# Kernel optimization log

Hardware: AMD Instinct MI355X
Metric: run time of the kernel (lower is better)

The kernel has to match this reference:

```python
import jax, jax.numpy as jnp
import numpy as np

B, N, DIM = 2, 2048, 1024
H, DH = 16, 64
DIM_INNER = H * DH
EPS = float(jnp.finfo(jnp.float32).eps)  # torch nn.RMSNorm default eps = finfo.eps
THETA = 10000.0


def setup_inputs() -> dict:
    key = jax.random.key(0)
    ks = jax.random.split(key, 6)
    s = 0.02
    tokens = jax.random.normal(ks[0], (B, N, DIM), dtype=jnp.float32)
    w_norm = jnp.ones((DIM,), jnp.float32)                      # prenorm RMSNorm weight
    w_q = jax.random.normal(ks[1], (DIM, DIM_INNER), jnp.float32) * s
    w_k = jax.random.normal(ks[2], (DIM, 3 * DIM_INNER), jnp.float32) * s
    w_v = jax.random.normal(ks[3], (DIM, 3 * DIM_INNER), jnp.float32) * s
    w_key_norms = jnp.ones((3, DH), jnp.float32)                # 3 key RMSNorms
    w_nested_knorm = jnp.ones((DH,), jnp.float32)
    w_out = jax.random.normal(ks[4], (DIM_INNER, DIM), jnp.float32) * s
    return {"tokens": tokens, "w_norm": w_norm, "w_q": w_q, "w_k": w_k,
            "w_v": w_v, "w_key_norms": w_key_norms,
            "w_nested_knorm": w_nested_knorm, "w_out": w_out}


def rmsnorm(x, w):
    var = jnp.mean(jnp.square(x), axis=-1, keepdims=True)
    return x * jax.lax.rsqrt(var + EPS) * w


def rope(x):
    # interleaved (GPT-J style) rotary, as in rotary_embedding_torch defaults
    n, d = x.shape[-2], x.shape[-1]
    inv_freq = 1.0 / (THETA ** (jnp.arange(0, d, 2, dtype=jnp.float32) / d))
    freqs = jnp.arange(n, dtype=jnp.float32)[:, None] * inv_freq   # (n, d/2)
    cos = jnp.repeat(jnp.cos(freqs), 2, axis=-1)                   # (n, d)
    sin = jnp.repeat(jnp.sin(freqs), 2, axis=-1)
    x1, x2 = x[..., ::2], x[..., 1::2]
    x_rot = jnp.stack((-x2, x1), axis=-1).reshape(x.shape)         # rotate_half
    return x * cos + x_rot * sin


def attend(q, k, v):
    # rotate_queries_with_cached_keys with equal lengths -> plain rotary on both
    q = rope(q)
    k = rope(k)
    d = q.shape[-1]
    scores = jnp.einsum('bhqd,bhkd->bhqk', q, k) / jnp.sqrt(jnp.float32(d))
    n = scores.shape[-1]
    causal = jnp.tril(jnp.ones((n, n), dtype=bool))
    scores = jnp.where(causal, scores, -jnp.inf)
    attn = jax.nn.softmax(scores, axis=-1)
    return jnp.einsum('bhqk,bhkd->bhqd', attn, v)


def reference(tokens, w_norm, w_q, w_k, w_v, w_key_norms, w_nested_knorm, w_out):
    b, n = tokens.shape[:2]
    x = rmsnorm(tokens, w_norm)                                    # prenorm
    q = (x @ w_q).reshape(b, n, H, DH).transpose(0, 2, 1, 3)       # (b,h,n,d)
    # chunk(3, dim=-1) then split heads -> (3,b,h,n,d)
    ks = (x @ w_k).reshape(b, n, 3, H, DH).transpose(2, 0, 3, 1, 4)
    vs = (x @ w_v).reshape(b, n, 3, H, DH).transpose(2, 0, 3, 1, 4)
    ks = rmsnorm(ks, w_key_norms[:, None, None, None, :])          # per-branch key norm
    # three parallel causal attentions sharing the same queries
    nq, nk, nv = jax.vmap(attend, in_axes=(None, 0, 0))(q, ks, vs)
    nk = rmsnorm(nk, w_nested_knorm)
    out = attend(nq, nk, nv)                                       # nested attention
    out = out.transpose(0, 2, 1, 3).reshape(b, n, DIM_INNER)       # merge heads
    return out @ w_out
```

## Files before the change

kernel.cpp:

```cpp
#include <hip/hip_runtime.h>
#include <hip/hip_bf16.h>
#include <stdint.h>

typedef unsigned short u16;
typedef __attribute__((ext_vector_type(8))) short short8;
typedef __attribute__((ext_vector_type(4))) float float4v;
typedef __attribute__((ext_vector_type(4))) unsigned int uint4v;

#define B_    2
#define N_    2048
#define DIM_  1024
#define H_    16
#define DH_   64
#define DI_   1024
#define EPS_  1.1920928955078125e-07f
#define LOG2_THETA 13.287712379549449f
#define SCL_  0.18033688011112042f

__device__ __forceinline__ float bf2f(u16 u) {
    union { unsigned int i; float f; } v; v.i = ((unsigned int)u) << 16; return v.f;
}
__device__ __forceinline__ u16 f2bf(float f) {
    union { float f; unsigned int i; } v; v.f = f;
    unsigned int r = v.i + 0x7fff + ((v.i >> 16) & 1);
    return (u16)(r >> 16);
}
__device__ __forceinline__ unsigned int cvtpk(float a, float b) {
    unsigned int r;
    asm("v_cvt_pk_bf16_f32 %0, %1, %2" : "=v"(r) : "v"(a), "v"(b));
    return r;
}
__device__ __forceinline__ int perm32(int n) {
    return (n & ~31) + (((n >> 2) & 3) * 8) + (((n >> 4) & 1) * 4) + (n & 3);
}

__global__ __launch_bounds__(256) void k_rmsnorm_x(
    const float* __restrict__ tok, const float* __restrict__ w, u16* __restrict__ xn) {
    int row = blockIdx.x;
    int t = threadIdx.x;
    const float* tr = tok + (size_t)row * DIM_;
    float vals[4];
    float ss = 0.f;
#pragma unroll
    for (int i = 0; i < 4; ++i) {
        float v = tr[t + i * 256];
        vals[i] = v; ss += v * v;
    }
#pragma unroll
    for (int o = 32; o; o >>= 1) ss += __shfl_xor(ss, o, 64);
    __shared__ float red[4];
    if ((t & 63) == 0) red[t >> 6] = ss;
    __syncthreads();
    ss = red[0] + red[1] + red[2] + red[3];
    float rs = rsqrtf(ss * (1.0f / DIM_) + EPS_);
    u16* orow = xn + (size_t)row * DIM_;
#pragma unroll
    for (int i = 0; i < 4; ++i) {
        int c = t + i * 256;
        orow[c] = f2bf(vals[i] * rs * w[c]);
    }
}

__global__ __launch_bounds__(256) void k_transpose(
    const float* __restrict__ src, u16* __restrict__ dst, int K, int N) {
    __shared__ float tile[32][33];
    int n0 = blockIdx.x * 32, k0 = blockIdx.y * 32;
    int tx = threadIdx.x, ty = threadIdx.y;
#pragma unroll
    for (int i = 0; i < 4; ++i)
        tile[ty + 8 * i][tx] = src[(size_t)(k0 + ty + 8 * i) * N + n0 + tx];
    __syncthreads();
#pragma unroll
    for (int i = 0; i < 4; ++i)
        dst[(size_t)(n0 + ty + 8 * i) * K + k0 + tx] = f2bf(tile[tx][ty + 8 * i]);
}

__global__ __launch_bounds__(256) void k_transpose_qkv(
    const float* __restrict__ w_q, const float* __restrict__ w_k,
    const float* __restrict__ w_v, u16* __restrict__ dst) {
    __shared__ float tile[32][33];
    int c0 = blockIdx.x * 32, k0 = blockIdx.y * 32;
    const float* src; int sN, sc0;
    if (c0 < 1024)      { src = w_q; sN = 1024; sc0 = c0; }
    else if (c0 < 4096) { src = w_k; sN = 3072; sc0 = c0 - 1024; }
    else                { src = w_v; sN = 3072; sc0 = c0 - 4096; }
    int tx = threadIdx.x, ty = threadIdx.y;
#pragma unroll
    for (int i = 0; i < 4; ++i)
        tile[ty + 8 * i][tx] = src[(size_t)(k0 + ty + 8 * i) * sN + sc0 + tx];
    __syncthreads();
#pragma unroll
    for (int i = 0; i < 4; ++i)
        dst[(size_t)(c0 + ty + 8 * i) * 1024 + k0 + tx] = f2bf(tile[tx][ty + 8 * i]);
}

__global__ __launch_bounds__(256) void k_transpose_v(
    const u16* __restrict__ QKVB, u16* __restrict__ Vt) {
    int y = blockIdx.y;
    int s = y >> 5;
    int b = (y >> 4) & 1;
    int h = y & 15;
    int n0 = blockIdx.x * 64;
    __shared__ u16 tile[64][72];
    int t = threadIdx.x;
#pragma unroll
    for (int i = 0; i < 2; ++i) {
        int idx = i * 256 + t;
        int row = idx >> 3, c = idx & 7;
        uint4v v = *(const uint4v*)(QKVB + ((size_t)(b * N_) + n0 + row) * 7168
                                        + 4096 + s * 1024 + h * 64 + c * 8);
        *(uint4v*)&tile[row][c * 8] = v;
    }
    __syncthreads();
    u16* out = Vt + (size_t)y * 64 * N_;
#pragma unroll
    for (int i = 0; i < 2; ++i) {
        int idx = i * 256 + t;
        int dh = idx >> 3, c = idx & 7;
#pragma unroll
        for (int j = 0; j < 8; ++j) {
            int n = c * 8 + j;
            out[(size_t)dh * N_ + n0 + perm32(n)] = tile[n][dh];
        }
    }
}

template <bool OUT_F32>
__global__ __launch_bounds__(256) void k_gemm_bt(
    const u16* __restrict__ A, const u16* __restrict__ Bt, void* __restrict__ Cv,
    int K, int Ncols) {
    __shared__ u16 As[128 * 32];
    __shared__ u16 Bs[128 * 32];
    int m0 = blockIdx.x * 128, n0 = blockIdx.y * 128;
    int t = threadIdx.x;
    int w = t >> 6, lane = t & 63, ln = lane & 15, quad = lane >> 4;
    int wm = w & 1, wn = w >> 1;
    float4v acc[4][4] = {};
    const u16* Ag = A + (size_t)m0 * K;
    const u16* Bg = Bt + (size_t)n0 * K;
    for (int k0 = 0; k0 < K; k0 += 32) {
        __syncthreads();
#pragma unroll
        for (int i = 0; i < 2; ++i) {
            int idx = i * 256 + t;
            int row = idx >> 2, kb = idx & 3;
            const u16* ga = Ag + (size_t)row * K + k0 + kb * 8;
            const u16* gb = Bg + (size_t)row * K + k0 + kb * 8;
            __builtin_amdgcn_global_load_lds(
                (const __attribute__((address_space(1))) void*)ga,
                (__attribute__((address_space(3))) void*)(As + idx * 8), 16, 0, 0);
            __builtin_amdgcn_global_load_lds(
                (const __attribute__((address_space(1))) void*)gb,
                (__attribute__((address_space(3))) void*)(Bs + idx * 8), 16, 0, 0);
        }
        asm volatile("s_waitcnt vmcnt(0)" ::: "memory");
        __syncthreads();
        short8 af[4], bfr[4];
#pragma unroll
        for (int mt = 0; mt < 4; ++mt)
            af[mt] = *(const short8*)(As + (wm * 64 + mt * 16 + ln) * 32 + quad * 8);
#pragma unroll
        for (int nt = 0; nt < 4; ++nt)
            bfr[nt] = *(const short8*)(Bs + (wn * 64 + nt * 16 + ln) * 32 + quad * 8);
#pragma unroll
        for (int mt = 0; mt < 4; ++mt)
#pragma unroll
            for (int nt = 0; nt < 4; ++nt)
                acc[mt][nt] = __builtin_amdgcn_mfma_f32_16x16x32_bf16(
                    af[mt], bfr[nt], acc[mt][nt], 0, 0, 0);
    }
#pragma unroll
    for (int mt = 0; mt < 4; ++mt)
#pragma unroll
        for (int nt = 0; nt < 4; ++nt)
#pragma unroll
            for (int r = 0; r < 4; ++r) {
                int row = m0 + wm * 64 + mt * 16 + quad * 4 + r;
                int col = n0 + wn * 64 + nt * 16 + ln;
                if (OUT_F32)
                    ((float*)Cv)[(size_t)row * Ncols + col] = acc[mt][nt][r];
                else
                    ((u16*)Cv)[(size_t)row * Ncols + col] = f2bf(acc[mt][nt][r]);
            }
}

__global__ __launch_bounds__(256) void k_rms_rope_k(
    u16* __restrict__ buf, const float* __restrict__ w,
    int row_stride, int col0, int nsets) {
    int vid = blockIdx.x * 4 + (threadIdx.x >> 6);
    int lane = threadIdx.x & 63;
    int h = vid % H_;
    int s = (vid / H_) % nsets;
    int row = vid / (H_ * nsets);
    int n = row & (N_ - 1);
    u16* p = buf + (size_t)row * row_stride + col0 + s * 1024 + h * 64;
    float x = bf2f(p[lane]);
    float ss = x * x;
#pragma unroll
    for (int o = 32; o; o >>= 1) ss += __shfl_xor(ss, o, 64);
    float rs = rsqrtf(ss * (1.0f / 64.0f) + EPS_);
    float xn = x * rs * w[s * 64 + lane];
    float partner = __shfl_xor(xn, 1, 64);
    float inv = exp2f(-(float)(lane & ~1) * (LOG2_THETA / 64.0f));
    float fr = (float)n * inv;
    float sv, cv;
    __sincosf(fr, &sv, &cv);
    float out = xn * cv + ((lane & 1) ? partner : -partner) * sv;
    p[lane] = f2bf(out);
}

__global__ __launch_bounds__(256, 3) void k_flash(
    const u16* __restrict__ Q, int q_stride,
    const u16* __restrict__ K, const u16* __restrict__ Vt,
    u16* __restrict__ O, u16* __restrict__ Ot,
    int kv_stride, int set_off, size_t o_set_stride) {
    int bh = blockIdx.x;
    int s = blockIdx.z;
    int b = bh >> 4, h = bh & 15;
    int t = threadIdx.x;
    int w = t >> 6, lane = t & 63, ln = lane & 15, quad = lane >> 4;
    int lnx = ln & 7;

    const u16* Qb  = Q + ((size_t)b * N_) * q_stride + h * 64;
    const u16* Kb  = K + ((size_t)b * N_) * kv_stride + (size_t)s * set_off + h * 64;
    const u16* Vtb = Vt + (size_t)((s * B_ + b) * H_ + h) * (64 * (size_t)N_);

    __shared__ u16 Ks[3][64][64];
    __shared__ u16 Vs[3][64][64];

    short8 ones;
#pragma unroll
    for (int j = 0; j < 8; ++j) ((u16*)&ones)[j] = 0x3F80;

    auto stage = [&](int kt0, int buf) {
        int k0 = kt0 * 64;
#pragma unroll
        for (int i = 0; i < 2; ++i) {
            int idx = i * 256 + t;
            int row = idx >> 3, c = idx & 7;
            int csrc = ((c ^ (row & 7)) * 8);
            const u16* ga = Kb + (size_t)(k0 + row) * kv_stride + csrc;
            __builtin_amdgcn_global_load_lds(
                (const __attribute__((address_space(1))) void*)ga,
                (__attribute__((address_space(3))) void*)&Ks[buf][row][c * 8], 16, 0, 0);
            const u16* gv = Vtb + (size_t)row * N_ + k0 + csrc;
            __builtin_amdgcn_global_load_lds(
                (const __attribute__((address_space(1))) void*)gv,
                (__attribute__((address_space(3))) void*)&Vs[buf][row][c * 8], 16, 0, 0);
        }
    };

    const int NQT = N_ / 128;
    int nhalf = (gridDim.y * 2 == NQT) ? 2 : 1;

    for (int half = 0; half < nhalf; ++half) {
        int qt = half ? blockIdx.y : (NQT - 1 - blockIdx.y);
        int q0 = qt * 128;
        int qw = q0 + w * 32;

        if (half) __syncthreads();

        short8 qf[2][2];
        float mrow[2];
        float4v accO[2][4] = {};
        float4v accL[2] = {};
#pragma unroll
        for (int g = 0; g < 2; ++g) {
            int qg = qw + g * 16;
            int tokn = qg + ln;
            short8 raw[2];
#pragma unroll
            for (int f = 0; f < 2; ++f)
                raw[f] = *(const short8*)(Qb + (size_t)tokn * q_stride + f * 32 + quad * 8);
            float qn = 0.f;
#pragma unroll
            for (int f = 0; f < 2; ++f)
#pragma unroll
                for (int j = 0; j < 8; ++j) {
                    float v = bf2f(((const u16*)&raw[f])[j]);
                    qn += v * v;
                }
            qn += __shfl_xor(qn, 16, 64);
            qn += __shfl_xor(qn, 32, 64);
            mrow[g] = sqrtf(qn) * (8.0f * SCL_) * 1.03f + 1e-6f;
#pragma unroll
            for (int f = 0; f < 2; ++f) {
                u16 out8[8];
                int dbase = f * 32 + quad * 8;
#pragma unroll
                for (int tp = 0; tp < 4; ++tp) {
                    int d = dbase + 2 * tp;
                    float inv = exp2f((float)d * (-LOG2_THETA / 64.0f));
                    float fr = (float)tokn * inv;
                    float sv, cv;
                    __sincosf(fr, &sv, &cv);
                    float x0 = bf2f(((const u16*)&raw[f])[2 * tp]);
                    float x1 = bf2f(((const u16*)&raw[f])[2 * tp + 1]);
                    out8[2 * tp]     = f2bf((x0 * cv - x1 * sv) * SCL_);
                    out8[2 * tp + 1] = f2bf((x1 * cv + x0 * sv) * SCL_);
                }
                qf[g][f] = *(const short8*)out8;
            }
        }

        int ntb = 2 * qt + 2;
        stage(0, 0);
        stage(1, 1);
        int cbuf = 0, sbuf = 2;

        for (int kt0 = 0; kt0 < ntb; ++kt0) {
            if (kt0 + 1 < ntb)
                asm volatile("s_waitcnt vmcnt(4)" ::: "memory");
            else
                asm volatile("s_waitcnt vmcnt(0)" ::: "memory");
            __syncthreads();
            if (kt0 + 2 < ntb) stage(kt0 + 2, sbuf);
            int buf = cbuf;
            cbuf = (cbuf == 2) ? 0 : cbuf + 1;
            sbuf = (sbuf == 2) ? 0 : sbuf + 1;
            int k0 = kt0 * 64;
            if (k0 > qw + 31) continue;

            short8 kf[4][2];
#pragma unroll
            for (int kt = 0; kt < 4; ++kt) {
                const u16* krow = &Ks[buf][kt * 16 + ln][0];
                kf[kt][0] = *(const short8*)(krow + ((quad ^ lnx) * 8));
                kf[kt][1] = *(const short8*)(krow + (((4 + quad) ^ lnx) * 8));
            }

            short8 pb[2][2];
#pragma unroll
            for (int g = 0; g < 2; ++g) {
                int qg = qw + g * 16;
                float4v st[4];
                __builtin_amdgcn_s_setprio(1);
#pragma unroll
                for (int kt = 0; kt < 4; ++kt) {
                    float4v sa = {-mrow[g], -mrow[g], -mrow[g], -mrow[g]};
                    sa = __builtin_amdgcn_mfma_f32_16x16x32_bf16(kf[kt][0], qf[g][0], sa, 0, 0, 0);
                    sa = __builtin_amdgcn_mfma_f32_16x16x32_bf16(kf[kt][1], qf[g][1], sa, 0, 0, 0);
                    st[kt] = sa;
                }
                __builtin_amdgcn_s_setprio(0);
                if (k0 + 63 <= qg) {
#pragma unroll
                    for (int c = 0; c < 2; ++c) {
                        uint4v pk;
#pragma unroll
                        for (int kt2 = 0; kt2 < 2; ++kt2) {
                            pk[kt2 * 2 + 0] = cvtpk(exp2f(st[c * 2 + kt2][0]),
                                                    exp2f(st[c * 2 + kt2][1]));
                            pk[kt2 * 2 + 1] = cvtpk(exp2f(st[c * 2 + kt2][2]),
                                                    exp2f(st[c * 2 + kt2][3]));
                        }
                        pb[g][c] = *(short8*)&pk;
                    }
                } else {
                    int qr = qg + ln;
#pragma unroll
                    for (int c = 0; c < 2; ++c) {
                        uint4v pk;
#pragma unroll
                        for (int kt2 = 0; kt2 < 2; ++kt2) {
                            int kt = c * 2 + kt2;
                            float e[4];
#pragma unroll
                            for (int r = 0; r < 4; ++r) {
                                int kg = k0 + kt * 16 + quad * 4 + r;
                                float arg = (kg <= qr) ? st[kt][r] : -1e30f;
                                e[r] = exp2f(arg);
                            }
                            pk[kt2 * 2 + 0] = cvtpk(e[0], e[1]);
                            pk[kt2 * 2 + 1] = cvtpk(e[2], e[3]);
                        }
                        pb[g][c] = *(short8*)&pk;
                    }
                }
            }

            __builtin_amdgcn_s_setprio(1);
#pragma unroll
            for (int dc = 0; dc < 4; ++dc) {
                const u16* vrow = &Vs[buf][dc * 16 + ln][0];
                short8 vf0 = *(const short8*)(vrow + ((quad ^ lnx) * 8));
                short8 vf1 = *(const short8*)(vrow + (((4 + quad) ^ lnx) * 8));
#pragma unroll
                for (int g = 0; g < 2; ++g) {
                    accO[g][dc] = __builtin_amdgcn_mfma_f32_16x16x32_bf16(vf0, pb[g][0], accO[g][dc], 0, 0, 0);
                    accO[g][dc] = __builtin_amdgcn_mfma_f32_16x16x32_bf16(vf1, pb[g][1], accO[g][dc], 0, 0, 0);
                }
            }
#pragma unroll
            for (int g = 0; g < 2; ++g) {
                accL[g] = __builtin_amdgcn_mfma_f32_16x16x32_bf16(ones, pb[g][0], accL[g], 0, 0, 0);
                accL[g] = __builtin_amdgcn_mfma_f32_16x16x32_bf16(ones, pb[g][1], accL[g], 0, 0, 0);
            }
            __builtin_amdgcn_s_setprio(0);
        }

#pragma unroll
        for (int g = 0; g < 2; ++g) {
            float rinv = 1.0f / accL[g][0];
            int qg = qw + g * 16;
            int qr = qg + ln;
            if (s == 2) {
                u16* Otb = Ot + (size_t)(b * H_ + h) * (64 * (size_t)N_);
                int pos = perm32(qr & (N_ - 1)) + (qr & ~(N_ - 1));
#pragma unroll
                for (int dc = 0; dc < 4; ++dc)
#pragma unroll
                    for (int r = 0; r < 4; ++r)
                        Otb[(size_t)(dc * 16 + quad * 4 + r) * N_ + pos] =
                            f2bf(accO[g][dc][r] * rinv);
            } else {
                u16* Ob = O + (size_t)s * o_set_stride + ((size_t)b * N_) * DI_ + h * 64;
#pragma unroll
                for (int dc = 0; dc < 4; ++dc) {
                    uint2 pk;
                    pk.x = cvtpk(accO[g][dc][0] * rinv, accO[g][dc][1] * rinv);
                    pk.y = cvtpk(accO[g][dc][2] * rinv, accO[g][dc][3] * rinv);
                    *(uint2*)(Ob + (size_t)qr * DI_ + dc * 16 + quad * 4) = pk;
                }
            }
        }
    }
}

extern "C" void kernel_launch(void* const* d_in, const int* in_sizes, int n_in,
                              void* d_out, int out_size, void* d_ws, size_t ws_size,
                              hipStream_t stream) {
    const float* tok     = (const float*)d_in[0];
    const float* w_norm  = (const float*)d_in[1];
    const float* w_q     = (const float*)d_in[2];
    const float* w_k     = (const float*)d_in[3];
    const float* w_v     = (const float*)d_in[4];
    const float* w_keyn  = (const float*)d_in[5];
    const float* w_nestk = (const float*)d_in[6];
    const float* w_o     = (const float*)d_in[7];

    char* ws = (char*)d_ws;
    const size_t MB = 1024 * 1024;
    u16* QKVB  = (u16*)(ws + 0 * MB);
    u16* VtB   = (u16*)(ws + 56 * MB);
    u16* NQKV  = (u16*)(ws + 80 * MB);
    u16* WQKVT = (u16*)(ws + 80 * MB);
    u16* NVt   = (u16*)(ws + 96 * MB);
    u16* XN    = (u16*)(ws + 96 * MB);
    u16* OUT2  = (u16*)(ws + 104 * MB);
    u16* WOT   = (u16*)(ws + 80 * MB);

    const size_t SET = (size_t)B_ * N_ * DI_;

    k_transpose_qkv<<<dim3(224, 32), dim3(32, 8), 0, stream>>>(w_q, w_k, w_v, WQKVT);

    k_rmsnorm_x<<<B_ * N_, 256, 0, stream>>>(tok, w_norm, XN);

    k_gemm_bt<false><<<dim3(32, 56), 256, 0, stream>>>(XN, WQKVT, QKVB, 1024, 7168);

    k_transpose_v<<<dim3(N_ / 64, 3 * B_ * H_), 256, 0, stream>>>(QKVB, VtB);

    k_rms_rope_k<<<(B_ * N_ * 3 * H_) / 4, 256, 0, stream>>>(QKVB, w_keyn, 7168, 1024, 3);

    k_flash<<<dim3(B_ * H_, N_ / 256, 3), 256, 0, stream>>>(
        QKVB, 7168, QKVB + 1024, VtB, NQKV, NVt, 7168, 1024, SET);

    k_rms_rope_k<<<(B_ * N_ * H_) / 4, 256, 0, stream>>>(NQKV + SET, w_nestk, 1024, 0, 1);

    k_flash<<<dim3(B_ * H_, N_ / 128, 1), 256, 0, stream>>>(
        NQKV, 1024, NQKV + SET, NVt, OUT2, NVt , 1024, 0, 0);

    k_transpose<<<dim3(32, 32), dim3(32, 8), 0, stream>>>(w_o, WOT, 1024, 1024);
    k_gemm_bt<true><<<dim3(32, 8), 256, 0, stream>>>(OUT2, WOT, (float*)d_out, 1024, 1024);
}
```

Baseline: 446.0 us.

## Software-pipeline attention loop: overlap PV of previous tile with QK/exp of current

Restructures the causal attention inner loop so that the P·V MFMAs for the previous key tile are issued after the QK MFMAs of the current tile and before its exp2 softmax work, letting matrix and vector ALU work interleave. It also cuts the global-to-LDS prefetch distance from two tiles to one, waiting on vmcnt(0) every iteration while still using three LDS buffers. The change is meant to hide exp latency behind MFMA, but it exposes more memory latency through the shallower prefetch and the full wait each iteration, and it keeps more live registers (st for both groups plus pb).

```diff
diff --git a/kernel.cpp b/kernel.cpp
--- a/kernel.cpp
+++ b/kernel.cpp
@@ -264,6 +264,7 @@
         float mrow[2];
         float4v accO[2][4] = {};
         float4v accL[2] = {};
+        short8 pb[2][2];
 #pragma unroll
         for (int g = 0; g < 2; ++g) {
             int qg = qw + g * 16;
@@ -303,86 +304,11 @@
             }
         }
 
-        int ntb = 2 * qt + 2;
-        stage(0, 0);
-        stage(1, 1);
-        int cbuf = 0, sbuf = 2;
-
-        for (int kt0 = 0; kt0 < ntb; ++kt0) {
-            if (kt0 + 1 < ntb)
-                asm volatile("s_waitcnt vmcnt(4)" ::: "memory");
-            else
-                asm volatile("s_waitcnt vmcnt(0)" ::: "memory");
-            __syncthreads();
-            if (kt0 + 2 < ntb) stage(kt0 + 2, sbuf);
-            int buf = cbuf;
-            cbuf = (cbuf == 2) ? 0 : cbuf + 1;
-            sbuf = (sbuf == 2) ? 0 : sbuf + 1;
-            int k0 = kt0 * 64;
-            if (k0 > qw + 31) continue;
-
-            short8 kf[4][2];
-#pragma unroll
-            for (int kt = 0; kt < 4; ++kt) {
-                const u16* krow = &Ks[buf][kt * 16 + ln][0];
-                kf[kt][0] = *(const short8*)(krow + ((quad ^ lnx) * 8));
-                kf[kt][1] = *(const short8*)(krow + (((4 + quad) ^ lnx) * 8));
-            }
-
-            short8 pb[2][2];
-#pragma unroll
-            for (int g = 0; g < 2; ++g) {
-                int qg = qw + g * 16;
-                float4v st[4];
-                __builtin_amdgcn_s_setprio(1);
-#pragma unroll
-                for (int kt = 0; kt < 4; ++kt) {
-                    float4v sa = {-mrow[g], -mrow[g], -mrow[g], -mrow[g]};
-                    sa = __builtin_amdgcn_mfma_f32_16x16x32_bf16(kf[kt][0], qf[g][0], sa, 0, 0, 0);
-                    sa = __builtin_amdgcn_mfma_f32_16x16x32_bf16(kf[kt][1], qf[g][1], sa, 0, 0, 0);
-                    st[kt] = sa;
-                }
-                __builtin_amdgcn_s_setprio(0);
-                if (k0 + 63 <= qg) {
-#pragma unroll
-                    for (int c = 0; c < 2; ++c) {
-                        uint4v pk;
-#pragma unroll
-                        for (int kt2 = 0; kt2 < 2; ++kt2) {
-                            pk[kt2 * 2 + 0] = cvtpk(exp2f(st[c * 2 + kt2][0]),
-                                                    exp2f(st[c * 2 + kt2][1]));
-                            pk[kt2 * 2 + 1] = cvtpk(exp2f(st[c * 2 + kt2][2]),
-                                                    exp2f(st[c * 2 + kt2][3]));
-                        }
-                        pb[g][c] = *(short8*)&pk;
-                    }
-                } else {
-                    int qr = qg + ln;
-#pragma unroll
-                    for (int c = 0; c < 2; ++c) {
-                        uint4v pk;
-#pragma unroll
-                        for (int kt2 = 0; kt2 < 2; ++kt2) {
-                            int kt = c * 2 + kt2;
-                            float e[4];
-#pragma unroll
-                            for (int r = 0; r < 4; ++r) {
-                                int kg = k0 + kt * 16 + quad * 4 + r;
-                                float arg = (kg <= qr) ? st[kt][r] : -1e30f;
-                                e[r] = exp2f(arg);
-                            }
-                            pk[kt2 * 2 + 0] = cvtpk(e[0], e[1]);
-                            pk[kt2 * 2 + 1] = cvtpk(e[2], e[3]);
-                        }
-                        pb[g][c] = *(short8*)&pk;
-                    }
-                }
-            }
-
+        auto do_pv = [&](int pbuf) {
             __builtin_amdgcn_s_setprio(1);
 #pragma unroll
             for (int dc = 0; dc < 4; ++dc) {
-                const u16* vrow = &Vs[buf][dc * 16 + ln][0];
+                const u16* vrow = &Vs[pbuf][dc * 16 + ln][0];
                 short8 vf0 = *(const short8*)(vrow + ((quad ^ lnx) * 8));
                 short8 vf1 = *(const short8*)(vrow + (((4 + quad) ^ lnx) * 8));
 #pragma unroll
@@ -397,7 +323,84 @@
                 accL[g] = __builtin_amdgcn_mfma_f32_16x16x32_bf16(ones, pb[g][1], accL[g], 0, 0, 0);
             }
             __builtin_amdgcn_s_setprio(0);
-        }
+        };
+
+        int ntb = 2 * qt + 2;
+        stage(0, 0);
+        int pend = -1;
+
+        for (int kt0 = 0; kt0 < ntb; ++kt0) {
+            asm volatile("s_waitcnt vmcnt(0)" ::: "memory");
+            __syncthreads();
+            if (kt0 + 1 < ntb) stage(kt0 + 1, (kt0 + 1) % 3);
+            int buf = kt0 % 3;
+            int k0 = kt0 * 64;
+            if (k0 <= qw + 31) {
+                short8 kf[4][2];
+#pragma unroll
+                for (int kt = 0; kt < 4; ++kt) {
+                    const u16* krow = &Ks[buf][kt * 16 + ln][0];
+                    kf[kt][0] = *(const short8*)(krow + ((quad ^ lnx) * 8));
+                    kf[kt][1] = *(const short8*)(krow + (((4 + quad) ^ lnx) * 8));
+                }
+                float4v st[2][4];
+                __builtin_amdgcn_s_setprio(1);
+#pragma unroll
+                for (int g = 0; g < 2; ++g)
+#pragma unroll
+                    for (int kt = 0; kt < 4; ++kt) {
+                        float4v sa = {-mrow[g], -mrow[g], -mrow[g], -mrow[g]};
+                        sa = __builtin_amdgcn_mfma_f32_16x16x32_bf16(kf[kt][0], qf[g][0], sa, 0, 0, 0);
+                        sa = __builtin_amdgcn_mfma_f32_16x16x32_bf16(kf[kt][1], qf[g][1], sa, 0, 0, 0);
+                        st[g][kt] = sa;
+                    }
+                __builtin_amdgcn_s_setprio(0);
+                if (pend >= 0) do_pv(pend % 3);
+#pragma unroll
+                for (int g = 0; g < 2; ++g) {
+                    int qg = qw + g * 16;
+                    if (k0 + 63 <= qg) {
+#pragma unroll
+                        for (int c = 0; c < 2; ++c) {
+                            uint4v pk;
+#pragma unroll
+                            for (int kt2 = 0; kt2 < 2; ++kt2) {
+                                pk[kt2 * 2 + 0] = cvtpk(exp2f(st[g][c * 2 + kt2][0]),
+                                                        exp2f(st[g][c * 2 + kt2][1]));
+                                pk[kt2 * 2 + 1] = cvtpk(exp2f(st[g][c * 2 + kt2][2]),
+                                                        exp2f(st[g][c * 2 + kt2][3]));
+                            }
+                            pb[g][c] = *(short8*)&pk;
+                        }
+                    } else {
+                        int qr = qg + ln;
+#pragma unroll
+                        for (int c = 0; c < 2; ++c) {
+                            uint4v pk;
+#pragma unroll
+                            for (int kt2 = 0; kt2 < 2; ++kt2) {
+                                int kt = c * 2 + kt2;
+                                float e[4];
+#pragma unroll
+                                for (int r = 0; r < 4; ++r) {
+                                    int kg = k0 + kt * 16 + quad * 4 + r;
+                                    float arg = (kg <= qr) ? st[g][kt][r] : -1e30f;
+                                    e[r] = exp2f(arg);
+                                }
+                                pk[kt2 * 2 + 0] = cvtpk(e[0], e[1]);
+                                pk[kt2 * 2 + 1] = cvtpk(e[2], e[3]);
+                            }
+                            pb[g][c] = *(short8*)&pk;
+                        }
+                    }
+                }
+                pend = kt0;
+            } else if (pend >= 0) {
+                do_pv(pend % 3);
+                pend = -1;
+            }
+        }
+        if (pend >= 0) do_pv(pend % 3);
 
 #pragma unroll
         for (int g = 0; g < 2; ++g) {
```

Result: slower. 465.1 us (+4.3%).
